# Kernel tuning notes

Hardware: AMD Instinct MI355X
Metric: run time of the kernel (lower is better)

The kernel has to match this reference:

```python
import jax, jax.numpy as jnp
import numpy as np

DIM_MODEL = 1024
HEADS = 16
DIM_PER_HEAD = DIM_MODEL // HEADS


def setup_inputs() -> dict:
    key = jax.random.key(0)
    k0, k1, k2, k3, k4 = jax.random.split(key, 5)
    x = jax.random.normal(k0, (2, 2048, DIM_MODEL), dtype=jnp.float32)
    # combined_linear: dim_model -> 3*dim_model (torch Linear: y = x @ W.T + b)
    s_in = 1.0 / np.sqrt(DIM_MODEL)
    W_qkv = jax.random.uniform(k1, (3 * DIM_MODEL, DIM_MODEL), minval=-s_in, maxval=s_in, dtype=jnp.float32)
    b_qkv = jax.random.uniform(k2, (3 * DIM_MODEL,), minval=-s_in, maxval=s_in, dtype=jnp.float32)
    W_out = jax.random.uniform(k3, (DIM_MODEL, DIM_MODEL), minval=-s_in, maxval=s_in, dtype=jnp.float32)
    b_out = jax.random.uniform(k4, (DIM_MODEL,), minval=-s_in, maxval=s_in, dtype=jnp.float32)
    return {"x": x, "W_qkv": W_qkv, "b_qkv": b_qkv, "W_out": W_out, "b_out": b_out}


def reference(x, W_qkv, b_qkv, W_out, b_out):
    B, S, D = x.shape
    H, Dh = HEADS, DIM_PER_HEAD
    qkv = x @ W_qkv.T + b_qkv  # [B, S, 3D]
    q, k, v = jnp.split(qkv, 3, axis=2)
    # [B, H, S, Dh]
    q = q.reshape(B, S, H, Dh).transpose(0, 2, 1, 3)
    k = k.reshape(B, S, H, Dh).transpose(0, 2, 1, 3)
    v = v.reshape(B, S, H, Dh).transpose(0, 2, 1, 3)
    scores = jnp.einsum('bhqd,bhkd->bhqk', q, k) / jnp.sqrt(jnp.float32(Dh))
    causal = jnp.tril(jnp.ones((S, S), dtype=bool))
    scores = jnp.where(causal[None, None, :, :], scores, -jnp.inf)
    p_attn = jax.nn.softmax(scores, axis=-1)
    out = jnp.einsum('bhqk,bhkd->bhqd', p_attn, v)
    out = out.transpose(0, 2, 1, 3).reshape(B, S, D)
    return out @ W_out.T + b_out
```

## Files before the change

kernel.cpp:

```cpp
#include <hip/hip_runtime.h>
#include <cstdint>

typedef __attribute__((ext_vector_type(8))) __bf16 bf16x8;
typedef __attribute__((ext_vector_type(4))) float f32x4;
typedef __attribute__((ext_vector_type(8))) short short8;
typedef __attribute__((ext_vector_type(4))) float float4v;
typedef __attribute__((ext_vector_type(4))) unsigned uint4v;
typedef __attribute__((ext_vector_type(4))) unsigned short ushort4v;

__device__ __forceinline__ unsigned short f2bf(float f) {
    unsigned u = __builtin_bit_cast(unsigned, f);
    u += 0x7fffu + ((u >> 16) & 1u);
    return (unsigned short)(u >> 16);
}
__device__ __forceinline__ float bf2f(unsigned short s) {
    return __builtin_bit_cast(float, (unsigned)s << 16);
}
__device__ __forceinline__ f32x4 mfma_bf16(bf16x8 a, bf16x8 b, f32x4 c) {
    return __builtin_amdgcn_mfma_f32_16x16x32_bf16(a, b, c, 0, 0, 0);
}
__device__ __forceinline__ unsigned pkbf(float lo, float hi) {
    unsigned r;
    asm("v_cvt_pk_bf16_f32 %0, %1, %2" : "=v"(r) : "v"(lo), "v"(hi));
    return r;
}

#define GLD16(g, l)                                                                     \
    __builtin_amdgcn_global_load_lds((const __attribute__((address_space(1))) void*)(g), \
                                     (__attribute__((address_space(3))) void*)(l), 16, 0, 0)

__global__ void __launch_bounds__(256) cvt_all(const float* __restrict__ x,
                                               const float* __restrict__ wqkv,
                                               const float* __restrict__ wout,
                                               unsigned short* __restrict__ xb,
                                               unsigned short* __restrict__ wqb,
                                               unsigned short* __restrict__ wob) {
    int i = blockIdx.x * blockDim.x + threadIdx.x;
#pragma unroll
    for (int k = 0; k < 2; k++, i += 524288) {
        const float* s;
        unsigned short* d;
        int off;
        if (i < 524288)      { s = x;    d = xb;  off = i; }
        else if (i < 917504) { s = wqkv; d = wqb; off = i - 524288; }
        else                 { s = wout; d = wob; off = i - 917504; }
        const float4v* sp = (const float4v*)(s + (size_t)off * 8);
        float4v v0 = sp[0], v1 = sp[1];
        uint4v u;
        u[0] = pkbf(v0[0], v0[1]);
        u[1] = pkbf(v0[2], v0[3]);
        u[2] = pkbf(v1[0], v1[1]);
        u[3] = pkbf(v1[2], v1[3]);
        *(uint4v*)(d + (size_t)off * 8) = u;
    }
}


#define STG_A(bf_, i_, t_) \
    GLD16(gA + (size_t)(i_) * 64 * 1024 + (size_t)(t_) * 64, (char*)&Asl[bf_][0] + (i_) * 8192 + w * 1024)
#define STG_B(bf_, i_, t_) \
    GLD16(gB + (size_t)(i_) * 64 * 1024 + (size_t)(t_) * 64, (char*)&Bsl[bf_][0] + (i_) * 8192 + w * 1024)

#define LDA(c_, mf_, kk_) \
    (*(const bf16x8*)((const char*)&Asl[c_][0] + (wm * 128 + (mf_) * 16 + a) * 128 + (((((kk_) << 2) + g) ^ xa) << 4)))
#define LDB(c_, nf_, kk_) \
    (*(const bf16x8*)((const char*)&Bsl[c_][0] + (wn * 48 + (nf_) * 16 + a) * 128 + (((((kk_) << 2) + g) ^ xa) << 4)))

#define PHASE(c_, mb_)                                                        \
    {                                                                         \
        bf16x8 a0_ = LDA(c_, mb_, 0), a1_ = LDA(c_, mb_, 1);                  \
        bf16x8 a2_ = LDA(c_, (mb_) + 1, 0), a3_ = LDA(c_, (mb_) + 1, 1);      \
        __builtin_amdgcn_s_setprio(1);                                        \
        _Pragma("unroll") for (int nf_ = 0; nf_ < 3; nf_++) {                 \
            acc[mb_][nf_]       = mfma_bf16(a0_, bfr[nf_][0], acc[mb_][nf_]);       \
            acc[mb_][nf_]       = mfma_bf16(a1_, bfr[nf_][1], acc[mb_][nf_]);       \
            acc[(mb_) + 1][nf_] = mfma_bf16(a2_, bfr[nf_][0], acc[(mb_) + 1][nf_]); \
            acc[(mb_) + 1][nf_] = mfma_bf16(a3_, bfr[nf_][1], acc[(mb_) + 1][nf_]); \
        }                                                                     \
        __builtin_amdgcn_s_setprio(0);                                        \
    }

__global__ void __launch_bounds__(512, 2) gemm_qkv(const unsigned short* __restrict__ A,
                                                   const unsigned short* __restrict__ B,
                                                   const float* __restrict__ bias,
                                                   unsigned short* __restrict__ qkbuf,
                                                   unsigned short* __restrict__ vT) {
    constexpr int K = 1024;
    __shared__ __attribute__((aligned(16))) unsigned short Asl[2][256 * 64];
    __shared__ __attribute__((aligned(16))) unsigned short Bsl[2][192 * 64];
    const int tid = threadIdx.x;
    const int w = tid >> 6, lane = tid & 63;
    const int a = lane & 15, g = lane >> 4;
    const int xa = a & 7;
    const int wm = w >> 2, wn = w & 3;

    const int nfb = ((int)blockIdx.x & 7) * 32 + ((int)blockIdx.x >> 3);
    const int bx = nfb >> 4, by = nfb & 15;
    const int m0 = by * 256, n0 = bx * 192;

    f32x4 acc[8][3];
#pragma unroll
    for (int i = 0; i < 8; i++)
#pragma unroll
        for (int j = 0; j < 3; j++) acc[i][j] = (f32x4)(0.0f);

    const int rA = tid >> 3, uA = tid & 7;
    const unsigned short* gA = A + (size_t)(m0 + rA) * K + ((uA ^ (rA & 7)) << 3);
    const unsigned short* gB = B + (size_t)(n0 + rA) * K + ((uA ^ (rA & 7)) << 3);

    STG_A(0, 0, 0); STG_A(0, 1, 0); STG_A(0, 2, 0); STG_A(0, 3, 0);
    STG_B(0, 0, 0); STG_B(0, 1, 0); STG_B(0, 2, 0);

    for (int t = 0; t < 16; ++t) {
        const int c = t & 1, nx = c ^ 1;
        const bool more = (t < 15);

        if (more) { STG_A(nx, 0, t + 1); STG_A(nx, 1, t + 1); }
        if (more) asm volatile("s_waitcnt vmcnt(2)" ::: "memory");
        else      asm volatile("s_waitcnt vmcnt(0)" ::: "memory");
        __builtin_amdgcn_s_barrier();

        bf16x8 bfr[3][2];
#pragma unroll
        for (int nf = 0; nf < 3; nf++) {
            bfr[nf][0] = LDB(c, nf, 0);
            bfr[nf][1] = LDB(c, nf, 1);
        }
        PHASE(c, 0);
        __builtin_amdgcn_s_barrier();

        if (more) { STG_A(nx, 2, t + 1); STG_A(nx, 3, t + 1); }
        PHASE(c, 2);
        __builtin_amdgcn_s_barrier();

        if (more) { STG_B(nx, 0, t + 1); STG_B(nx, 1, t + 1); }
        PHASE(c, 4);
        __builtin_amdgcn_s_barrier();

        if (more) { STG_B(nx, 2, t + 1); }
        PHASE(c, 6);
        asm volatile("" ::: "memory");
        __builtin_amdgcn_s_barrier();
    }

#pragma unroll
    for (int nf = 0; nf < 3; nf++) {
        const int cb = n0 + wn * 48 + nf * 16;
        const int col = cb + a;
        const float bv = bias[col];
        if (cb < 2048) {
#pragma unroll
            for (int mf = 0; mf < 8; mf++)
#pragma unroll
                for (int jr = 0; jr < 4; jr++) {
                    const int row = m0 + wm * 128 + mf * 16 + g * 4 + jr;
                    qkbuf[(size_t)row * 2048 + col] = f2bf(acc[mf][nf][jr] + bv);
                }
        } else {
            const int vd = col - 2048, hh = vd >> 6, dd = vd & 63;
#pragma unroll
            for (int mf = 0; mf < 8; mf++) {
                const int t0 = m0 + wm * 128 + mf * 16 + g * 4;
                const int bb = t0 >> 11, kl = t0 & 2047;
                ushort4v st;
#pragma unroll
                for (int jr = 0; jr < 4; jr++) st[jr] = f2bf(acc[mf][nf][jr] + bv);
                *(ushort4v*)(vT + ((size_t)((bb << 4) + hh) * 64 + dd) * 2048 + kl) = st;
            }
        }
    }
}

__global__ void __launch_bounds__(256) gemm_bt(const unsigned short* __restrict__ A,
                                               const unsigned short* __restrict__ B,
                                               const float* __restrict__ bias,
                                               float* __restrict__ C,
                                               int M, int N, int K) {
    __shared__ __attribute__((aligned(16))) unsigned short As[2][128 * 32];
    __shared__ __attribute__((aligned(16))) unsigned short Bs[2][128 * 32];
    const int tid = threadIdx.x;
    const int w = tid >> 6, lane = tid & 63;
    const int a = lane & 15, g = lane >> 4;

    const int cpx = gridDim.x >> 3;
    const int nf = ((int)blockIdx.x & 7) * cpx + ((int)blockIdx.x >> 3);
    const int bx = nf >> 5;
    const int by = nf & 31;
    const int m0 = by * 128, n0 = bx * 128;
    const int wr = (w >> 1) * 64, wc = (w & 1) * 64;

    f32x4 acc[4][4];
#pragma unroll
    for (int i = 0; i < 4; i++)
#pragma unroll
        for (int j = 0; j < 4; j++) acc[i][j] = (f32x4)(0.0f);

    const int r0 = tid >> 2;
    const int c0 = (tid & 3) * 8;
    const unsigned short* gA0 = A + (size_t)(m0 + r0) * K + c0;
    const unsigned short* gA1 = A + (size_t)(m0 + 64 + r0) * K + c0;
    const unsigned short* gB0 = B + (size_t)(n0 + r0) * K + c0;
    const unsigned short* gB1 = B + (size_t)(n0 + 64 + r0) * K + c0;

#define GSTAGE(buf_, k0_)                                               \
    {                                                                   \
        char* la_ = (char*)&As[buf_][0] + w * 1024;                     \
        char* lb_ = (char*)&Bs[buf_][0] + w * 1024;                     \
        GLD16(gA0 + (k0_), la_);                                        \
        GLD16(gA1 + (k0_), la_ + 4096);                                 \
        GLD16(gB0 + (k0_), lb_);                                        \
        GLD16(gB1 + (k0_), lb_ + 4096);                                 \
    }

    GSTAGE(0, 0);
    __syncthreads();

    int cur = 0;
    for (int k0 = 0; k0 < K; k0 += 32) {
        if (k0 + 32 < K) GSTAGE(cur ^ 1, k0 + 32);

        bf16x8 af[4], bfr[4];
#pragma unroll
        for (int i = 0; i < 4; i++) {
            af[i]  = *(const bf16x8*)&As[cur][(wr + i * 16 + a) * 32 + g * 8];
            bfr[i] = *(const bf16x8*)&Bs[cur][(wc + i * 16 + a) * 32 + g * 8];
        }
#pragma unroll
        for (int i = 0; i < 4; i++)
#pragma unroll
            for (int j = 0; j < 4; j++) acc[i][j] = mfma_bf16(af[i], bfr[j], acc[i][j]);

        __syncthreads();
        cur ^= 1;
    }
#undef GSTAGE

#pragma unroll
    for (int j = 0; j < 4; j++) {
        const int col = n0 + wc + j * 16 + a;
        const float bv = bias[col];
#pragma unroll
        for (int i = 0; i < 4; i++)
#pragma unroll
            for (int jr = 0; jr < 4; jr++) {
                const int row = m0 + wr + i * 16 + g * 4 + jr;
                C[(size_t)row * N + col] = acc[i][j][jr] + bv;
            }
    }
}


#define STAGE(bf_, t_)                                                  \
    {                                                                   \
        const size_t ko_ = (size_t)(t_) * 128 * LDQ;                    \
        const size_t vo_ = (size_t)(t_) * 128;                          \
        char* db_ = (char*)&KV[bf_][0] + w * 1024;                      \
        GLD16(sK0 + ko_, db_);                                          \
        GLD16(sK1 + ko_, db_ + 8192);                                   \
        GLD16(sV0 + vo_, db_ + 16384);                                  \
        GLD16(sV1 + vo_, db_ + 24576);                                  \
    }

__global__ void __launch_bounds__(512, 4) attn_fwd(const unsigned short* __restrict__ qk,
                                                   const unsigned short* __restrict__ vT,
                                                   unsigned short* __restrict__ o) {
    constexpr int SL = 2048, DH = 64, LDQ = 2048;
    constexpr float GAMMA = 0.18033688011112042f;
    const int bh = blockIdx.x & 31;
    const int s = blockIdx.x >> 5;
    const int qb = (s < 8) ? 15 - s : s - 8;
    const int b = bh >> 4, h = bh & 15;
    const int tid = threadIdx.x;
    const int w = tid >> 6, lane = tid & 63;
    const int n = lane & 15, g = lane >> 4;

    __shared__ __attribute__((aligned(16))) unsigned short KV[2][16384];

    const int qs = qb * 128 + w * 16 + n;
    const int nt = qb + 1;

    bf16x8 qf[2];
    {
        const unsigned short* qp = qk + (size_t)(b * SL + qs) * LDQ + h * DH + g * 8;
        short8 la = *(const short8*)qp, lb = *(const short8*)(qp + 32);
        short8 s0, s1;
#pragma unroll
        for (int e = 0; e < 8; e++) {
            s0[e] = (short)f2bf(bf2f((unsigned short)la[e]) * GAMMA);
            s1[e] = (short)f2bf(bf2f((unsigned short)lb[e]) * GAMMA);
        }
        qf[0] = __builtin_bit_cast(bf16x8, s0);
        qf[1] = __builtin_bit_cast(bf16x8, s1);
    }

    const int rK = tid >> 3;
    const int xrK = (rK & 3) | (((rK >> 3) & 1) << 2);
    const int csK = (((tid & 7) ^ xrK) << 3);
    const unsigned short* sK0 = qk + (size_t)(b * SL + rK) * LDQ + 1024 + h * DH + csK;
    const unsigned short* sK1 = sK0 + (size_t)64 * LDQ;
    const int dV = tid >> 4;
    const int csV = (((tid & 15) ^ (dV & 7)) << 3);
    const unsigned short* sV0 = vT + (size_t)bh * DH * SL + (size_t)dV * SL + csV;
    const unsigned short* sV1 = sV0 + (size_t)32 * SL;

    const int srow = 8 * (n >> 2) + (n & 3);
    const int xrq = (n & 3) | (((n >> 2) & 1) << 2);
    const int offK0 = ((g ^ xrq) << 3);
    const int offK1 = offK0 ^ 32;
    int offV[4];
#pragma unroll
    for (int kc = 0; kc < 4; kc++) offV[kc] = (((4 * kc + g) ^ (n & 7)) << 3);

    f32x4 of[4];
#pragma unroll
    for (int i = 0; i < 4; i++) of[i] = (f32x4)(0.0f);
    float m_i = -1e30f, l_i = 0.0f;

    STAGE(0, 0);
    __syncthreads();

    for (int t = 0; t < nt; ++t) {
        const unsigned short* kvb = &KV[t & 1][0];
        if (t + 1 < nt) STAGE((t & 1) ^ 1, t + 1);

        f32x4 p[8];
        __builtin_amdgcn_s_setprio(1);
#pragma unroll
        for (int f = 0; f < 8; f++) {
            const int r_ = srow + ((f >> 1) << 5) + ((f & 1) << 2);
            const bf16x8 ka_ = *(const bf16x8*)&kvb[r_ * 64 + offK0];
            const bf16x8 kc_ = *(const bf16x8*)&kvb[r_ * 64 + offK1];
            f32x4 acc_ = (f32x4)(0.0f);
            acc_ = mfma_bf16(ka_, qf[0], acc_);
            acc_ = mfma_bf16(kc_, qf[1], acc_);
            p[f] = acc_;
        }
        __builtin_amdgcn_s_setprio(0);

        if (t == nt - 1) {
            const int k0 = t * 128;
#pragma unroll
            for (int f = 0; f < 8; f++) {
                const int kb_ = k0 + ((f >> 1) << 5) + ((f & 1) << 2) + 8 * g;
#pragma unroll
                for (int e = 0; e < 4; e++)
                    if (kb_ + e > qs) p[f][e] = -1e30f;
            }
        }

        float mx = -1e30f;
#pragma unroll
        for (int f = 0; f < 8; f++) {
            const float a_ = fmaxf(fmaxf(p[f][0], p[f][1]), fmaxf(p[f][2], p[f][3]));
            mx = fmaxf(mx, a_);
        }
        mx = fmaxf(mx, __shfl_xor(mx, 16));
        mx = fmaxf(mx, __shfl_xor(mx, 32));
        if (!__all(mx <= m_i + 8.0f)) {
            const float mn_ = fmaxf(m_i, mx);
            const float al_ = __builtin_amdgcn_exp2f(m_i - mn_);
            l_i *= al_;
#pragma unroll
            for (int d_ = 0; d_ < 4; d_++) of[d_] = of[d_] * al_;
            m_i = mn_;
        }
        float rs = 0.0f;
#pragma unroll
        for (int f = 0; f < 8; f++)
#pragma unroll
            for (int e = 0; e < 4; e++) {
                p[f][e] = __builtin_amdgcn_exp2f(p[f][e] - m_i);
                rs += p[f][e];
            }
        l_i += rs;

        bf16x8 pf[4];
#pragma unroll
        for (int kc = 0; kc < 4; kc++) {
            uint4v u_;
            u_[0] = pkbf(p[2 * kc][0], p[2 * kc][1]);
            u_[1] = pkbf(p[2 * kc][2], p[2 * kc][3]);
            u_[2] = pkbf(p[2 * kc + 1][0], p[2 * kc + 1][1]);
            u_[3] = pkbf(p[2 * kc + 1][2], p[2 * kc + 1][3]);
            pf[kc] = __builtin_bit_cast(bf16x8, u_);
        }

        const unsigned short* vb = kvb + 8192;
        __builtin_amdgcn_s_setprio(1);
#pragma unroll
        for (int df = 0; df < 4; df++) {
            const int vrow = (df * 16 + n) * 128;
#pragma unroll
            for (int kc = 0; kc < 4; kc++) {
                const bf16x8 va_ = *(const bf16x8*)&vb[vrow + offV[kc]];
                of[df] = mfma_bf16(va_, pf[kc], of[df]);
            }
        }
        __builtin_amdgcn_s_setprio(0);

        __syncthreads();
    }

    float rl = l_i;
    rl += __shfl_xor(rl, 16);
    rl += __shfl_xor(rl, 32);
    const float inv = 1.0f / rl;
    unsigned short* op = o + (size_t)(b * SL + qs) * 1024 + h * DH + 4 * g;
#pragma unroll
    for (int df = 0; df < 4; df++) {
        ushort4v st;
#pragma unroll
        for (int r = 0; r < 4; r++) st[r] = f2bf(of[df][r] * inv);
        *(ushort4v*)(op + df * 16) = st;
    }
}

extern "C" void kernel_launch(void* const* d_in, const int* in_sizes, int n_in,
                              void* d_out, int out_size, void* d_ws, size_t ws_size,
                              hipStream_t stream) {
    (void)in_sizes; (void)n_in; (void)out_size; (void)ws_size;
    const float* x    = (const float*)d_in[0];
    const float* Wqkv = (const float*)d_in[1];
    const float* bqkv = (const float*)d_in[2];
    const float* Wout = (const float*)d_in[3];
    const float* bout = (const float*)d_in[4];
    float* out = (float*)d_out;

    const int BS = 2, SL = 2048, DM = 1024;
    const int M = BS * SL;
    const int K = DM;

    char* ws = (char*)d_ws;
    unsigned short* x_bf    = (unsigned short*)(ws);
    unsigned short* wqkv_bf = (unsigned short*)(ws + (8u << 20));
    unsigned short* wout_bf = (unsigned short*)(ws + (14u << 20));
    unsigned short* qkbuf   = (unsigned short*)(ws + (16u << 20));
    unsigned short* vTbuf   = (unsigned short*)(ws + (32u << 20));
    unsigned short* attn_o  = (unsigned short*)(ws + (40u << 20));

    cvt_all<<<2048, 256, 0, stream>>>(x, Wqkv, Wout, x_bf, wqkv_bf, wout_bf);

    gemm_qkv<<<dim3(256), 512, 0, stream>>>(x_bf, wqkv_bf, bqkv, qkbuf, vTbuf);

    attn_fwd<<<dim3(512), 512, 0, stream>>>(qkbuf, vTbuf, attn_o);

    gemm_bt<<<dim3(256), 256, 0, stream>>>(attn_o, wout_bf, bout, out, M, DM, K);
}
```

Baseline: 115.4 us.

## Restructure QKV GEMM main loop to issue LDS reads before global prefetch and barriers

```diff
diff --git a/kernel.cpp b/kernel.cpp
--- a/kernel.cpp
+++ b/kernel.cpp
@@ -66,19 +66,15 @@
 #define LDB(c_, nf_, kk_) \
     (*(const bf16x8*)((const char*)&Bsl[c_][0] + (wn * 48 + (nf_) * 16 + a) * 128 + (((((kk_) << 2) + g) ^ xa) << 4)))
 
-#define PHASE(c_, mb_)                                                        \
-    {                                                                         \
-        bf16x8 a0_ = LDA(c_, mb_, 0), a1_ = LDA(c_, mb_, 1);                  \
-        bf16x8 a2_ = LDA(c_, (mb_) + 1, 0), a3_ = LDA(c_, (mb_) + 1, 1);      \
-        __builtin_amdgcn_s_setprio(1);                                        \
-        _Pragma("unroll") for (int nf_ = 0; nf_ < 3; nf_++) {                 \
-            acc[mb_][nf_]       = mfma_bf16(a0_, bfr[nf_][0], acc[mb_][nf_]);       \
-            acc[mb_][nf_]       = mfma_bf16(a1_, bfr[nf_][1], acc[mb_][nf_]);       \
-            acc[(mb_) + 1][nf_] = mfma_bf16(a2_, bfr[nf_][0], acc[(mb_) + 1][nf_]); \
-            acc[(mb_) + 1][nf_] = mfma_bf16(a3_, bfr[nf_][1], acc[(mb_) + 1][nf_]); \
-        }                                                                     \
-        __builtin_amdgcn_s_setprio(0);                                        \
-    }
+#define MFMA12(mb_)                                                               \
+    __builtin_amdgcn_s_setprio(1);                                                \
+    _Pragma("unroll") for (int nf_ = 0; nf_ < 3; nf_++) {                         \
+        acc[mb_][nf_]       = mfma_bf16(a0_, bfr[nf_][0], acc[mb_][nf_]);         \
+        acc[mb_][nf_]       = mfma_bf16(a1_, bfr[nf_][1], acc[mb_][nf_]);         \
+        acc[(mb_) + 1][nf_] = mfma_bf16(a2_, bfr[nf_][0], acc[(mb_) + 1][nf_]);   \
+        acc[(mb_) + 1][nf_] = mfma_bf16(a3_, bfr[nf_][1], acc[(mb_) + 1][nf_]);   \
+    }                                                                             \
+    __builtin_amdgcn_s_setprio(0);
 
 __global__ void __launch_bounds__(512, 2) gemm_qkv(const unsigned short* __restrict__ A,
                                                    const unsigned short* __restrict__ B,
@@ -115,9 +111,7 @@
         const int c = t & 1, nx = c ^ 1;
         const bool more = (t < 15);
 
-        if (more) { STG_A(nx, 0, t + 1); STG_A(nx, 1, t + 1); }
-        if (more) asm volatile("s_waitcnt vmcnt(2)" ::: "memory");
-        else      asm volatile("s_waitcnt vmcnt(0)" ::: "memory");
+        asm volatile("s_waitcnt vmcnt(0)" ::: "memory");
         __builtin_amdgcn_s_barrier();
 
         bf16x8 bfr[3][2];
@@ -126,21 +120,47 @@
             bfr[nf][0] = LDB(c, nf, 0);
             bfr[nf][1] = LDB(c, nf, 1);
         }
-        PHASE(c, 0);
-        __builtin_amdgcn_s_barrier();
-
-        if (more) { STG_A(nx, 2, t + 1); STG_A(nx, 3, t + 1); }
-        PHASE(c, 2);
-        __builtin_amdgcn_s_barrier();
-
-        if (more) { STG_B(nx, 0, t + 1); STG_B(nx, 1, t + 1); }
-        PHASE(c, 4);
-        __builtin_amdgcn_s_barrier();
-
-        if (more) { STG_B(nx, 2, t + 1); }
-        PHASE(c, 6);
-        asm volatile("" ::: "memory");
-        __builtin_amdgcn_s_barrier();
+
+        {
+            bf16x8 a0_ = LDA(c, 0, 0), a1_ = LDA(c, 0, 1);
+            bf16x8 a2_ = LDA(c, 1, 0), a3_ = LDA(c, 1, 1);
+            if (more) { STG_A(nx, 0, t + 1); STG_A(nx, 1, t + 1); }
+            asm volatile("" ::: "memory");
+            __builtin_amdgcn_s_barrier();
+            asm volatile("s_waitcnt lgkmcnt(0)");
+            MFMA12(0);
+            __builtin_amdgcn_s_barrier();
+        }
+        {
+            bf16x8 a0_ = LDA(c, 2, 0), a1_ = LDA(c, 2, 1);
+            bf16x8 a2_ = LDA(c, 3, 0), a3_ = LDA(c, 3, 1);
+            if (more) { STG_A(nx, 2, t + 1); STG_A(nx, 3, t + 1); }
+            asm volatile("" ::: "memory");
+            __builtin_amdgcn_s_barrier();
+            asm volatile("s_waitcnt lgkmcnt(0)");
+            MFMA12(2);
+            __builtin_amdgcn_s_barrier();
+        }
+        {
+            bf16x8 a0_ = LDA(c, 4, 0), a1_ = LDA(c, 4, 1);
+            bf16x8 a2_ = LDA(c, 5, 0), a3_ = LDA(c, 5, 1);
+            if (more) { STG_B(nx, 0, t + 1); STG_B(nx, 1, t + 1); }
+            asm volatile("" ::: "memory");
+            __builtin_amdgcn_s_barrier();
+            asm volatile("s_waitcnt lgkmcnt(0)");
+            MFMA12(4);
+            __builtin_amdgcn_s_barrier();
+        }
+        {
+            bf16x8 a0_ = LDA(c, 6, 0), a1_ = LDA(c, 6, 1);
+            bf16x8 a2_ = LDA(c, 7, 0), a3_ = LDA(c, 7, 1);
+            if (more) { STG_B(nx, 2, t + 1); }
+            asm volatile("" ::: "memory");
+            __builtin_amdgcn_s_barrier();
+            asm volatile("s_waitcnt lgkmcnt(0)");
+            MFMA12(6);
+            __builtin_amdgcn_s_barrier();
+        }
     }
 
 #pragma unroll
```

Result: faster. 102.9 us (-10.8%).
